# Kernel tuning notes

Hardware: AMD Instinct MI355X
Metric: run time of the kernel (lower is better)

## Reference

```python
import jax, jax.numpy as jnp
import numpy as np

CHANNEL = 1
ALPHA = 1.0
EPS = 1e-10
SHAPE = (1, CHANNEL, 160, 192, 160)


def _sobel_kernels(channel):
    s2 = np.array([[-1., 0., 1.], [-2., 0., 2.], [-1., 0., 1.]], dtype=np.float32)
    # sobel.repeat(channel,1,3,1,1): 2D kernel tiled along depth -> k[d,h,w] = s2[h,w]
    kx = np.tile(s2[None, :, :], (3, 1, 1))
    ky = np.tile(s2.T[None, :, :], (3, 1, 1))
    kz = np.array([[[-1., -1., -1.], [-2., -2., -2.], [-1., -1., -1.]],
                   [[0., 0., 0.], [0., 0., 0.], [0., 0., 0.]],
                   [[1., 1., 1.], [2., 2., 2.], [1., 1., 1.]]], dtype=np.float32)
    def rep(k):  # -> [channel, 1, 3, 3, 3] for depthwise conv
        return jnp.asarray(np.tile(k[None, None], (channel, 1, 1, 1, 1)))
    return rep(kx), rep(ky), rep(kz)


def _conv3d(x, k, channel):
    # torch F.conv3d (cross-correlation), padding=1, groups=channel
    return jax.lax.conv_general_dilated(
        x, k, window_strides=(1, 1, 1), padding=((1, 1), (1, 1), (1, 1)),
        dimension_numbers=('NCDHW', 'OIDHW', 'NCDHW'),
        feature_group_count=channel)


def setup_inputs() -> dict:
    key = jax.random.key(0)
    k1, k2, k3 = jax.random.split(key, 3)
    M = jax.random.normal(k1, SHAPE, dtype=jnp.float32)
    S = jax.random.normal(k2, SHAPE, dtype=jnp.float32)
    flow = jax.random.normal(k3, (SHAPE[0], 3) + SHAPE[2:], dtype=jnp.float32)
    return {"M": M, "S": S, "flow": flow}


def reference(M, S, flow):
    kx, ky, kz = _sobel_kernels(CHANNEL)
    Idiff = M - S
    Sx = _conv3d(S, kx, CHANNEL)
    Sy = _conv3d(S, ky, CHANNEL)
    Sz = _conv3d(S, kz, CHANNEL)
    Mx = _conv3d(M, kx, CHANNEL)
    My = _conv3d(M, ky, CHANNEL)
    Mz = _conv3d(M, kz, CHANNEL)
    Sxyz_mag = Sx ** 2 + Sy ** 2 + Sz ** 2
    Mxyz_mag = Mx ** 2 + My ** 2 + Mz ** 2
    denom_S = Sxyz_mag + (ALPHA ** 2) * Idiff ** 2 + 1e-10
    denom_M = Mxyz_mag + (ALPHA ** 2) * Idiff ** 2 + 1e-10
    Ux = Idiff * (Sx / denom_S + Mx / denom_M)
    Uy = Idiff * (Sy / denom_S + My / denom_M)
    Uz = Idiff * (Sz / denom_S + Mz / denom_M)
    demons_ori_xz = jnp.arctan(Ux / (Uz + EPS))
    demons_ori_yz = jnp.arctan(Uy / (Uz + EPS))
    flow_ori_xz = jnp.arctan(flow[:, 0] / (flow[:, 2] + EPS))
    flow_ori_yz = jnp.arctan(flow[:, 1] / (flow[:, 2] + EPS))
    ori_error = jnp.mean((flow_ori_xz - demons_ori_xz) ** 2) + \
                jnp.mean((flow_ori_yz - demons_ori_yz) ** 2)
    return ori_error
```

## Files before the change

kernel.cpp:

```cpp
#include <hip/hip_runtime.h>
#include <math.h>

#define DD 160
#define HH 192
#define WW 160
#define TW 32
#define THB 16
#define TD 8
#define HW (HH * WW)
#define NVOX (DD * HW)
#define HTW 34
#define HTH 18
#define LSTR 34
#define HALO (HTH * HTW)

typedef float v2f __attribute__((ext_vector_type(2)));

__device__ __forceinline__ v2f vrcp(v2f a) {
    v2f r;
    r.x = __builtin_amdgcn_rcpf(a.x);
    r.y = __builtin_amdgcn_rcpf(a.y);
    return r;
}

__device__ __forceinline__ v2f atanv(v2f r) {
    v2f ar = __builtin_elementwise_abs(r);
    v2f inv = vrcp(ar);
    v2f x = __builtin_elementwise_min(ar, inv);
    v2f x2 = x * x;
    v2f p = __builtin_elementwise_fma(x2,
            __builtin_elementwise_fma(x2,
            __builtin_elementwise_fma(x2,
            __builtin_elementwise_fma(x2,
            __builtin_elementwise_fma(x2, (v2f)(-0.0117212f), (v2f)(0.05265332f)),
            (v2f)(-0.11643287f)), (v2f)(0.19354346f)), (v2f)(-0.33262347f)),
            (v2f)(0.99997726f));
    p *= x;
    v2f q = 1.57079632679489662f - p;
    v2f res;
    res.x = ar.x > 1.0f ? q.x : p.x;
    res.y = ar.y > 1.0f ? q.y : p.y;
    res.x = copysignf(res.x, r.x);
    res.y = copysignf(res.y, r.y);
    return res;
}

__global__ __launch_bounds__(256) void demons_ori_kernel(
    const float* __restrict__ Mv, const float* __restrict__ Sv,
    const float* __restrict__ flow, float* __restrict__ out)
{
    __shared__ float buf[2][2][HTH * LSTR];
    __shared__ float redbuf[4];

    const int tid = threadIdx.x;
    const int lane = tid & 63;
    const int wid = tid >> 6;
    const int tw = lane & 31;
    const int r  = wid * 4 + (lane >> 5) * 2;
    const int w0 = blockIdx.x * TW;
    const int h0 = blockIdx.y * THB;
    const int d0 = blockIdx.z * TD;

    const bool has2 = (tid < HALO - 512);
    int gb0, gb1, gb2 = 0;
    bool ok0, ok1, ok2 = false;
    {
        int i = tid;
        int hh = i / HTW, ww = i - HTW * hh;
        int gh = h0 + hh - 1, gw = w0 + ww - 1;
        ok0 = (gh >= 0 && gh < HH && gw >= 0 && gw < WW);
        gb0 = gh * WW + gw;
        i = tid + 256;
        hh = i / HTW; ww = i - HTW * hh;
        gh = h0 + hh - 1; gw = w0 + ww - 1;
        ok1 = (gh >= 0 && gh < HH && gw >= 0 && gw < WW);
        gb1 = gh * WW + gw;
        if (has2) {
            i = tid + 512;
            hh = i / HTW; ww = i - HTW * hh;
            gh = h0 + hh - 1; gw = w0 + ww - 1;
            ok2 = (gh >= 0 && gh < HH && gw >= 0 && gw < WW);
            gb2 = gh * WW + gw;
        }
    }

    float pS0 = 0.f, pM0 = 0.f, pS1 = 0.f, pM1 = 0.f, pS2 = 0.f, pM2 = 0.f;

    auto issue = [&](int d) {
        const bool din = (d >= 0) && (d < DD);
        const size_t base = (size_t)d * HW;
        pS0 = (din && ok0) ? Sv[base + gb0] : 0.f;
        pM0 = (din && ok0) ? Mv[base + gb0] : 0.f;
        pS1 = (din && ok1) ? Sv[base + gb1] : 0.f;
        pM1 = (din && ok1) ? Mv[base + gb1] : 0.f;
        pS2 = (din && ok2) ? Sv[base + gb2] : 0.f;
        pM2 = (din && ok2) ? Mv[base + gb2] : 0.f;
    };
    auto commit = [&](int d) {
        float* __restrict__ bS = &buf[d & 1][0][0];
        float* __restrict__ bM = &buf[d & 1][1][0];
        bS[tid] = pS0;        bM[tid] = pM0;
        bS[tid + 256] = pS1;  bM[tid + 256] = pM1;
        if (has2) { bS[tid + 512] = pS2; bM[tid + 512] = pM2; }
    };

    const int rb = r * LSTR + tw;
    auto fieldPartials = [&](const float* __restrict__ b,
                             v2f& Px, v2f& Py, v2f& Bq, v2f& Cq) {
        const float* r0 = b + rb;
        const float* r1 = r0 + LSTR;
        const float* r2 = r1 + LSTR;
        const float* r3 = r2 + LSTR;
        float a0 = r0[0], b0 = r0[1], c0 = r0[2];
        float a1 = r1[0], b1 = r1[1], c1 = r1[2];
        float a2 = r2[0], b2 = r2[1], c2 = r2[2];
        float a3 = r3[0], b3 = r3[1], c3 = r3[2];
        float X0 = c0 - a0, X1 = c1 - a1, X2 = c2 - a2, X3 = c3 - a3;
        float W0 = a0 + 2.f * b0 + c0, W1 = a1 + 2.f * b1 + c1;
        float W2 = a2 + 2.f * b2 + c2, W3 = a3 + 2.f * b3 + c3;
        float I0 = a0 + b0 + c0, I1 = a1 + b1 + c1;
        float I2 = a2 + b2 + c2, I3 = a3 + b3 + c3;
        Px = (v2f){X0 + 2.f * X1 + X2, X1 + 2.f * X2 + X3};
        Py = (v2f){W2 - W0, W3 - W1};
        Bq = (v2f){I0 + 2.f * I1 + I2, I1 + 2.f * I2 + I3};
        Cq = (v2f){b1, b2};
    };

    v2f mSPx, mSPy, mSB, mSC, mMPx, mMPy, mMB, mMC;
    v2f zSPx, zSPy, zSB, zSC, zMPx, zMPy, zMB, zMC;
    v2f pSPx, pSPy, pSB, pSC, pMPx, pMPy, pMB, pMC;

    issue(d0 - 1);
    commit(d0 - 1);
    issue(d0);
    __syncthreads();
    fieldPartials(&buf[(d0 - 1) & 1][0][0], mSPx, mSPy, mSB, mSC);
    fieldPartials(&buf[(d0 - 1) & 1][1][0], mMPx, mMPy, mMB, mMC);
    commit(d0);
    issue(d0 + 1);
    __syncthreads();
    fieldPartials(&buf[d0 & 1][0][0], zSPx, zSPy, zSB, zSC);
    fieldPartials(&buf[d0 & 1][1][0], zMPx, zMPy, zMB, zMC);

    const size_t voffA = (size_t)(h0 + r) * WW + (w0 + tw);
    v2f fFx, fFy, fFz;
    {
        size_t o = (size_t)d0 * HW + voffA;
        fFx = (v2f){flow[o], flow[o + WW]};
        fFy = (v2f){flow[NVOX + o], flow[NVOX + o + WW]};
        fFz = (v2f){flow[2 * (size_t)NVOX + o], flow[2 * (size_t)NVOX + o + WW]};
    }

    v2f vsum = (v2f){0.f, 0.f};

    #pragma unroll
    for (int dd = 0; dd < TD; ++dd) {
        const int d = d0 + dd;
        commit(d + 1);
        v2f nFx = (v2f){0.f, 0.f}, nFy = nFx, nFz = nFx;
        if (dd < TD - 1) {
            issue(d + 2);
            size_t o = (size_t)(d + 1) * HW + voffA;
            nFx = (v2f){flow[o], flow[o + WW]};
            nFy = (v2f){flow[NVOX + o], flow[NVOX + o + WW]};
            nFz = (v2f){flow[2 * (size_t)NVOX + o], flow[2 * (size_t)NVOX + o + WW]};
        }
        __syncthreads();
        fieldPartials(&buf[(d + 1) & 1][0][0], pSPx, pSPy, pSB, pSC);
        fieldPartials(&buf[(d + 1) & 1][1][0], pMPx, pMPy, pMB, pMC);

        v2f idf = zMC - zSC;
        v2f i2  = __builtin_elementwise_fma(idf, idf, (v2f)(1e-10f));
        v2f gxS = mSPx + zSPx + pSPx;
        v2f gyS = mSPy + zSPy + pSPy;
        v2f gzS = pSB - mSB;
        v2f gxM = mMPx + zMPx + pMPx;
        v2f gyM = mMPy + zMPy + pMPy;
        v2f gzM = pMB - mMB;
        v2f denS = __builtin_elementwise_fma(gxS, gxS,
                   __builtin_elementwise_fma(gyS, gyS,
                   __builtin_elementwise_fma(gzS, gzS, i2)));
        v2f denM = __builtin_elementwise_fma(gxM, gxM,
                   __builtin_elementwise_fma(gyM, gyM,
                   __builtin_elementwise_fma(gzM, gzM, i2)));
        v2f rS = vrcp(denS);
        v2f rM = vrcp(denM);
        v2f Ux = idf * __builtin_elementwise_fma(gxS, rS, gxM * rM);
        v2f Uy = idf * __builtin_elementwise_fma(gyS, rS, gyM * rM);
        v2f Uz = idf * __builtin_elementwise_fma(gzS, rS, gzM * rM);
        v2f rz = vrcp(Uz + 1e-10f);
        v2f dxz = atanv(Ux * rz);
        v2f dyz = atanv(Uy * rz);

        v2f rf = vrcp(fFz + 1e-10f);
        v2f fxz = atanv(fFx * rf);
        v2f fyz = atanv(fFy * rf);

        v2f e1 = fxz - dxz;
        v2f e2 = fyz - dyz;
        vsum = __builtin_elementwise_fma(e1, e1,
               __builtin_elementwise_fma(e2, e2, vsum));

        mSPx = zSPx; mSPy = zSPy; mSB = zSB; mSC = zSC;
        mMPx = zMPx; mMPy = zMPy; mMB = zMB; mMC = zMC;
        zSPx = pSPx; zSPy = pSPy; zSB = pSB; zSC = pSC;
        zMPx = pMPx; zMPy = pMPy; zMB = pMB; zMC = pMC;
        fFx = nFx; fFy = nFy; fFz = nFz;
    }

    float lsum = vsum.x + vsum.y;
    #pragma unroll
    for (int o = 32; o > 0; o >>= 1)
        lsum += __shfl_down(lsum, o, 64);
    if (lane == 0)
        redbuf[wid] = lsum;
    __syncthreads();
    if (tid == 0) {
        float s = redbuf[0] + redbuf[1] + redbuf[2] + redbuf[3];
        atomicAdd(out, s * (1.0f / (float)NVOX));
    }
}

extern "C" void kernel_launch(void* const* d_in, const int* in_sizes, int n_in,
                              void* d_out, int out_size, void* d_ws, size_t ws_size,
                              hipStream_t stream) {
    const float* Mv   = (const float*)d_in[0];
    const float* Sv   = (const float*)d_in[1];
    const float* flow = (const float*)d_in[2];
    float* out = (float*)d_out;

    hipMemsetAsync(out, 0, sizeof(float), stream);

    dim3 grid(WW / TW, HH / THB, DD / TD);
    demons_ori_kernel<<<grid, dim3(256), 0, stream>>>(Mv, Sv, flow, out);
}
```

Measured before the change: 129.9 us.

## Compute atan of ratios via min/max form and halve depth tile

```diff
diff --git a/kernel.cpp b/kernel.cpp
--- a/kernel.cpp
+++ b/kernel.cpp
@@ -6,7 +6,7 @@
 #define WW 160
 #define TW 32
 #define THB 16
-#define TD 8
+#define TD 4
 #define HW (HH * WW)
 #define NVOX (DD * HW)
 #define HTW 34
@@ -23,10 +23,12 @@
     return r;
 }
 
-__device__ __forceinline__ v2f atanv(v2f r) {
-    v2f ar = __builtin_elementwise_abs(r);
-    v2f inv = vrcp(ar);
-    v2f x = __builtin_elementwise_min(ar, inv);
+__device__ __forceinline__ v2f atan_ratio(v2f num, v2f den) {
+    v2f a = __builtin_elementwise_abs(num);
+    v2f b = __builtin_elementwise_abs(den);
+    v2f mn = __builtin_elementwise_min(a, b);
+    v2f mx = __builtin_elementwise_max(a, b);
+    v2f x = mn * vrcp(mx);
     v2f x2 = x * x;
     v2f p = __builtin_elementwise_fma(x2,
             __builtin_elementwise_fma(x2,
@@ -38,10 +40,12 @@
     p *= x;
     v2f q = 1.57079632679489662f - p;
     v2f res;
-    res.x = ar.x > 1.0f ? q.x : p.x;
-    res.y = ar.y > 1.0f ? q.y : p.y;
-    res.x = copysignf(res.x, r.x);
-    res.y = copysignf(res.y, r.y);
+    res.x = a.x > b.x ? q.x : p.x;
+    res.y = a.y > b.y ? q.y : p.y;
+    unsigned sx = (__float_as_uint(num.x) ^ __float_as_uint(den.x)) & 0x80000000u;
+    unsigned sy = (__float_as_uint(num.y) ^ __float_as_uint(den.y)) & 0x80000000u;
+    res.x = __uint_as_float(__float_as_uint(res.x) | sx);
+    res.y = __uint_as_float(__float_as_uint(res.y) | sy);
     return res;
 }
 
@@ -188,13 +192,14 @@
         v2f Ux = idf * __builtin_elementwise_fma(gxS, rS, gxM * rM);
         v2f Uy = idf * __builtin_elementwise_fma(gyS, rS, gyM * rM);
         v2f Uz = idf * __builtin_elementwise_fma(gzS, rS, gzM * rM);
-        v2f rz = vrcp(Uz + 1e-10f);
-        v2f dxz = atanv(Ux * rz);
-        v2f dyz = atanv(Uy * rz);
-
-        v2f rf = vrcp(fFz + 1e-10f);
-        v2f fxz = atanv(fFx * rf);
-        v2f fyz = atanv(fFy * rf);
+
+        v2f uzp = Uz + 1e-10f;
+        v2f dxz = atan_ratio(Ux, uzp);
+        v2f dyz = atan_ratio(Uy, uzp);
+
+        v2f fzp = fFz + 1e-10f;
+        v2f fxz = atan_ratio(fFx, fzp);
+        v2f fyz = atan_ratio(fFy, fzp);
 
         v2f e1 = fxz - dxz;
         v2f e2 = fyz - dyz;
```

After: 139.8 us. 7.6% more time.
